# Performance work log

Measured on AMD Instinct MI355X. Metric: run time of the kernel, lower is better.

Reference implementation:

```python
import jax, jax.numpy as jnp
import numpy as np

B, D_IN, D_H = 32768, 512, 512


def setup_inputs() -> dict:
    key = jax.random.key(0)
    ks = jax.random.split(key, 7)
    s_in = 1.0 / np.sqrt(D_IN)
    s_h = 1.0 / np.sqrt(D_H)
    x = jax.random.normal(ks[0], (B, D_IN), dtype=jnp.float32)
    C = jax.random.normal(ks[1], (B, D_H), dtype=jnp.float32)
    h = jax.random.normal(ks[2], (B, D_H), dtype=jnp.float32)
    # Concatenated gate weights: order [i, f, o, g]. Each gate has its own
    # independent Linear(input_dim->hidden) and Linear(hidden->hidden) in torch;
    # stacking them column-wise gives identical math with 2 GEMMs.
    Wx = jax.random.uniform(ks[3], (D_IN, 4 * D_H), dtype=jnp.float32, minval=-s_in, maxval=s_in)
    bx = jax.random.uniform(ks[4], (4 * D_H,), dtype=jnp.float32, minval=-s_in, maxval=s_in)
    Wh = jax.random.uniform(ks[5], (D_H, 4 * D_H), dtype=jnp.float32, minval=-s_h, maxval=s_h)
    bh = jax.random.uniform(ks[6], (4 * D_H,), dtype=jnp.float32, minval=-s_h, maxval=s_h)
    return {"x": x, "C": C, "h": h, "Wx": Wx, "bx": bx, "Wh": Wh, "bh": bh}


def reference(x, C, h, Wx, bx, Wh, bh):
    # Two fused GEMMs replace the 8 small Linear calls (same math).
    z = x @ Wx + bx + h @ Wh + bh  # [B, 4H]
    i, f, o, g = jnp.split(z, 4, axis=-1)
    i = jax.nn.sigmoid(i)
    f = jax.nn.sigmoid(f)
    o = jax.nn.sigmoid(o)
    g = jnp.tanh(g)
    C_new = f * C + i * g
    h_new = o * jnp.tanh(C_new)
    return (C_new, h_new)
```

## Files before the change

### kernel.cpp

```cpp
#include <hip/hip_runtime.h>
#include <stdint.h>


#define BROWS 32768
#define DH 512
#define KTOT 1024
#define BM 128
#define BK 64

typedef __attribute__((ext_vector_type(8))) __bf16 bf16x8;
typedef __attribute__((ext_vector_type(4))) float f32x4;

__device__ __forceinline__ float sigf(float v)  { return 1.0f / (1.0f + __expf(-v)); }
__device__ __forceinline__ float tanhf_(float v){ return 1.0f - 2.0f / (1.0f + __expf(2.0f * v)); }

__global__ void pack_w(const float* __restrict__ Wx, const float* __restrict__ Wh,
                       __bf16* __restrict__ Wt) {
  int o  = blockIdx.x * 256 + threadIdx.x;
  int k  = o & (KTOT - 1);
  int rg = o >> 10;
  int jb = rg >> 7;
  int r  = rg & 127;
  int g  = (r >> 4) & 3;
  int hl = ((r >> 6) << 4) | (r & 15);
  int n  = g * DH + jb * 32 + hl;
  float v = (k < DH) ? Wx[k * 4 * DH + n] : Wh[(k - DH) * 4 * DH + n];
  Wt[o] = (__bf16)v;
}

__global__ __launch_bounds__(256, 3) void lstm_gemm(
    const float* __restrict__ x, const float* __restrict__ h,
    const __bf16* __restrict__ Wt, const float* __restrict__ bx,
    const float* __restrict__ bh, const float* __restrict__ Cin,
    float* __restrict__ out) {
  __shared__ __attribute__((aligned(16))) __bf16 As[BM * BK];
  __shared__ __attribute__((aligned(16))) __bf16 Bs[BM * BK];

  const int tid  = threadIdx.x;
  const int lane = tid & 63;
  const int wave = tid >> 6;
  const int wm = wave >> 1, wn = wave & 1;
  const int jb   = blockIdx.x;
  const int bm   = blockIdx.y;
  const int row0 = bm * BM;

  const __bf16* Bt = Wt + (size_t)jb * 128 * KTOT;

  f32x4 acc[4][4];
  #pragma unroll
  for (int a_ = 0; a_ < 4; ++a_)
    #pragma unroll
    for (int b_ = 0; b_ < 4; ++b_) acc[a_][b_] = (f32x4)0.0f;

  for (int k0 = 0; k0 < KTOT; k0 += BK) {
    const float* Aptr = (k0 < DH) ? (x + (size_t)row0 * DH + k0)
                                  : (h + (size_t)row0 * DH + (k0 - DH));
    bf16x8 ta[4], tb[4];
    #pragma unroll
    for (int it = 0; it < 4; ++it) {
      int lin = it * 256 + tid;
      int r = lin >> 3, c8 = lin & 7;
      const float* src = Aptr + r * DH + c8 * 8;
      float4 f0 = *(const float4*)src;
      float4 f1 = *(const float4*)(src + 4);
      bf16x8 v;
      v[0] = (__bf16)f0.x; v[1] = (__bf16)f0.y;
      v[2] = (__bf16)f0.z; v[3] = (__bf16)f0.w;
      v[4] = (__bf16)f1.x; v[5] = (__bf16)f1.y;
      v[6] = (__bf16)f1.z; v[7] = (__bf16)f1.w;
      ta[it] = v;
    }
    #pragma unroll
    for (int it = 0; it < 4; ++it) {
      int lin = it * 256 + tid;
      int r = lin >> 3, c8 = lin & 7;
      tb[it] = *(const bf16x8*)(Bt + (size_t)r * KTOT + k0 + c8 * 8);
    }
    #pragma unroll
    for (int it = 0; it < 4; ++it) {
      int lin = it * 256 + tid;
      *(bf16x8*)&As[lin * 8] = ta[it];
      *(bf16x8*)&Bs[lin * 8] = tb[it];
    }
    __syncthreads();

    #pragma unroll
    for (int ks = 0; ks < 2; ++ks) {
      const int ko = ks * 32 + (lane >> 4) * 8;
      bf16x8 af[4], bfr[4];
      #pragma unroll
      for (int cm = 0; cm < 4; ++cm)
        af[cm] = *(const bf16x8*)&As[(wm * 64 + cm * 16 + (lane & 15)) * BK + ko];
      #pragma unroll
      for (int cn = 0; cn < 4; ++cn)
        bfr[cn] = *(const bf16x8*)&Bs[(wn * 64 + cn * 16 + (lane & 15)) * BK + ko];
      #pragma unroll
      for (int cm = 0; cm < 4; ++cm)
        #pragma unroll
        for (int cn = 0; cn < 4; ++cn)
          acc[cm][cn] = __builtin_amdgcn_mfma_f32_16x16x32_bf16(
              af[cm], bfr[cn], acc[cm][cn], 0, 0, 0);
    }
    __syncthreads();
  }

  const int hd = jb * 32 + wn * 16 + (lane & 15);
  float bias[4];
  #pragma unroll
  for (int g2 = 0; g2 < 4; ++g2)
    bias[g2] = bx[g2 * DH + hd] + bh[g2 * DH + hd];

  #pragma unroll
  for (int cm = 0; cm < 4; ++cm) {
    const int rbase = row0 + wm * 64 + cm * 16 + (lane >> 4) * 4;
    #pragma unroll
    for (int i2 = 0; i2 < 4; ++i2) {
      const size_t r = (size_t)(rbase + i2);
      float ig = sigf(acc[cm][0][i2] + bias[0]);
      float fg = sigf(acc[cm][1][i2] + bias[1]);
      float og = sigf(acc[cm][2][i2] + bias[2]);
      float gg = tanhf_(acc[cm][3][i2] + bias[3]);
      float cp = Cin[r * DH + hd];
      float cnew = fg * cp + ig * gg;
      float hnew = og * tanhf_(cnew);
      out[r * DH + hd] = cnew;
      out[(size_t)BROWS * DH + r * DH + hd] = hnew;
    }
  }
}

__global__ void lstm_naive(const float* __restrict__ x, const float* __restrict__ Cin,
                           const float* __restrict__ h, const float* __restrict__ Wx,
                           const float* __restrict__ bxp, const float* __restrict__ Wh,
                           const float* __restrict__ bhp, float* __restrict__ out) {
  int idx = blockIdx.x * 256 + threadIdx.x;
  int r = idx >> 9, hd = idx & 511;
  float z[4];
  #pragma unroll
  for (int g = 0; g < 4; ++g)
    z[g] = bxp[g * DH + hd] + bhp[g * DH + hd];
  for (int k = 0; k < DH; ++k) {
    float xv = x[(size_t)r * DH + k];
    #pragma unroll
    for (int g = 0; g < 4; ++g) z[g] += xv * Wx[k * 4 * DH + g * DH + hd];
  }
  for (int k = 0; k < DH; ++k) {
    float hv = h[(size_t)r * DH + k];
    #pragma unroll
    for (int g = 0; g < 4; ++g) z[g] += hv * Wh[k * 4 * DH + g * DH + hd];
  }
  float ig = sigf(z[0]), fg = sigf(z[1]), og = sigf(z[2]), gg = tanhf_(z[3]);
  float cp = Cin[(size_t)r * DH + hd];
  float cnew = fg * cp + ig * gg;
  float hnew = og * tanhf_(cnew);
  out[(size_t)r * DH + hd] = cnew;
  out[(size_t)BROWS * DH + (size_t)r * DH + hd] = hnew;
}

extern "C" void kernel_launch(void* const* d_in, const int* in_sizes, int n_in,
                              void* d_out, int out_size, void* d_ws, size_t ws_size,
                              hipStream_t stream) {
  const float* x  = (const float*)d_in[0];
  const float* Ci = (const float*)d_in[1];
  const float* h  = (const float*)d_in[2];
  const float* Wx = (const float*)d_in[3];
  const float* bx = (const float*)d_in[4];
  const float* Wh = (const float*)d_in[5];
  const float* bh = (const float*)d_in[6];
  float* out = (float*)d_out;

  const size_t need = (size_t)2048 * KTOT * sizeof(__bf16);
  if (ws_size >= need) {
    __bf16* Wt = (__bf16*)d_ws;
    pack_w<<<dim3((2048 * KTOT) / 256), dim3(256), 0, stream>>>(Wx, Wh, Wt);
    lstm_gemm<<<dim3(16, 256), dim3(256), 0, stream>>>(x, h, Wt, bx, bh, Ci, out);
  } else {
    lstm_naive<<<dim3((BROWS * DH) / 256), dim3(256), 0, stream>>>(
        x, Ci, h, Wx, bx, Wh, bh, out);
  }
}
```

Before: 505.0 us.

## Pre-convert activations to bf16 and load GEMM tiles directly into LDS

Adds a pre-pass that converts x and h to one concatenated bf16 buffer. The main GEMM then loads its tiles with global_load_lds straight into an XOR-swizzled LDS layout, which should cut bank conflicts and register staging. Cin is prefetched before the K loop, and pack_w is rewritten with an LDS transpose so its global reads coalesce. The cost is an extra pass that reads fp32 activations and writes a 64MB workspace buffer, and the new path only runs when the workspace is large enough.

```diff
diff --git a/kernel.cpp b/kernel.cpp
--- a/kernel.cpp
+++ b/kernel.cpp
@@ -10,22 +10,154 @@
 
 typedef __attribute__((ext_vector_type(8))) __bf16 bf16x8;
 typedef __attribute__((ext_vector_type(4))) float f32x4;
+typedef __attribute__((address_space(1))) void gvoid;
+typedef __attribute__((address_space(3))) void lvoid;
+
+__device__ __forceinline__ void gl_lds16(const void* g, void* l) {
+  __builtin_amdgcn_global_load_lds((gvoid*)g, (lvoid*)l, 16, 0, 0);
+}
 
 __device__ __forceinline__ float sigf(float v)  { return 1.0f / (1.0f + __expf(-v)); }
 __device__ __forceinline__ float tanhf_(float v){ return 1.0f - 2.0f / (1.0f + __expf(2.0f * v)); }
 
+__global__ void conv_xh(const float* __restrict__ x, const float* __restrict__ h,
+                        __bf16* __restrict__ xh) {
+  int o = blockIdx.x * 256 + threadIdx.x;
+  int c = (o & 127) * 8;
+  int r = o >> 7;
+  const float* src = (c < DH) ? (x + (size_t)r * DH + c)
+                              : (h + (size_t)r * DH + (c - DH));
+  float4 f0 = *(const float4*)src;
+  float4 f1 = *(const float4*)(src + 4);
+  bf16x8 v;
+  v[0] = (__bf16)f0.x; v[1] = (__bf16)f0.y; v[2] = (__bf16)f0.z; v[3] = (__bf16)f0.w;
+  v[4] = (__bf16)f1.x; v[5] = (__bf16)f1.y; v[6] = (__bf16)f1.z; v[7] = (__bf16)f1.w;
+  *(bf16x8*)(xh + (size_t)o * 8) = v;
+}
+
 __global__ void pack_w(const float* __restrict__ Wx, const float* __restrict__ Wh,
                        __bf16* __restrict__ Wt) {
-  int o  = blockIdx.x * 256 + threadIdx.x;
-  int k  = o & (KTOT - 1);
-  int rg = o >> 10;
-  int jb = rg >> 7;
-  int r  = rg & 127;
-  int g  = (r >> 4) & 3;
-  int hl = ((r >> 6) << 4) | (r & 15);
-  int n  = g * DH + jb * 32 + hl;
-  float v = (k < DH) ? Wx[k * 4 * DH + n] : Wh[(k - DH) * 4 * DH + n];
-  Wt[o] = (__bf16)v;
+  __shared__ __bf16 T[128][72];
+  const int jb = blockIdx.y;
+  const int k0 = blockIdx.x * 64;
+  const float* Wsrc = (k0 < DH) ? (Wx + (size_t)k0 * 4 * DH)
+                                : (Wh + (size_t)(k0 - DH) * 4 * DH);
+  const int t = threadIdx.x;
+  const int s = t & 31, kr0 = t >> 5;
+  const int g = s >> 3, q = s & 7;
+  const int r0 = (q >> 2) * 64 + g * 16 + (q & 3) * 4;
+  #pragma unroll
+  for (int it = 0; it < 8; ++it) {
+    int kr = it * 8 + kr0;
+    float4 f = *(const float4*)(Wsrc + (size_t)kr * 4 * DH + g * DH + jb * 32 + q * 4);
+    T[r0 + 0][kr] = (__bf16)f.x;
+    T[r0 + 1][kr] = (__bf16)f.y;
+    T[r0 + 2][kr] = (__bf16)f.z;
+    T[r0 + 3][kr] = (__bf16)f.w;
+  }
+  __syncthreads();
+  #pragma unroll
+  for (int it = 0; it < 4; ++it) {
+    int lin = it * 256 + t;
+    int r = lin >> 3, k8 = lin & 7;
+    bf16x8 v;
+    #pragma unroll
+    for (int j = 0; j < 8; ++j) v[j] = T[r][k8 * 8 + j];
+    *(bf16x8*)(Wt + (size_t)(jb * 128 + r) * KTOT + k0 + k8 * 8) = v;
+  }
+}
+
+__global__ __launch_bounds__(256, 3) void lstm_gemm2(
+    const __bf16* __restrict__ xh, const __bf16* __restrict__ Wt,
+    const float* __restrict__ bx, const float* __restrict__ bh,
+    const float* __restrict__ Cin, float* __restrict__ out) {
+  __shared__ __attribute__((aligned(16))) __bf16 As[BM * BK];
+  __shared__ __attribute__((aligned(16))) __bf16 Bs[BM * BK];
+
+  const int tid  = threadIdx.x;
+  const int lane = tid & 63;
+  const int wave = tid >> 6;
+  const int wm = wave >> 1, wn = wave & 1;
+  const int jb   = blockIdx.x;
+  const int row0 = blockIdx.y * BM;
+
+  const __bf16* Bt = Wt + (size_t)jb * 128 * KTOT;
+
+  const int hd = jb * 32 + wn * 16 + (lane & 15);
+  float bias[4], cpv[4][4];
+  #pragma unroll
+  for (int g = 0; g < 4; ++g) bias[g] = bx[g * DH + hd] + bh[g * DH + hd];
+  #pragma unroll
+  for (int cm = 0; cm < 4; ++cm)
+    #pragma unroll
+    for (int i2 = 0; i2 < 4; ++i2)
+      cpv[cm][i2] = Cin[(size_t)(row0 + wm * 64 + cm * 16 + (lane >> 4) * 4 + i2) * DH + hd];
+
+  f32x4 acc[4][4];
+  #pragma unroll
+  for (int a_ = 0; a_ < 4; ++a_)
+    #pragma unroll
+    for (int b_ = 0; b_ < 4; ++b_) acc[a_][b_] = (f32x4)0.0f;
+
+  for (int k0 = 0; k0 < KTOT; k0 += BK) {
+    #pragma unroll
+    for (int it = 0; it < 4; ++it) {
+      int lin = it * 256 + tid;
+      int r = lin >> 3, c8 = lin & 7;
+      int cs = c8 ^ (r & 7);
+      gl_lds16(xh + (size_t)(row0 + r) * KTOT + k0 + cs * 8, &As[lin * 8]);
+    }
+    #pragma unroll
+    for (int it = 0; it < 4; ++it) {
+      int lin = it * 256 + tid;
+      int r = lin >> 3, c8 = lin & 7;
+      int cs = c8 ^ (r & 7);
+      gl_lds16(Bt + (size_t)r * KTOT + k0 + cs * 8, &Bs[lin * 8]);
+    }
+    __syncthreads();
+
+    #pragma unroll
+    for (int ks = 0; ks < 2; ++ks) {
+      const int q = lane >> 4;
+      bf16x8 af[4], bfr[4];
+      #pragma unroll
+      for (int cm = 0; cm < 4; ++cm) {
+        int row = wm * 64 + cm * 16 + (lane & 15);
+        int cc = (ks * 4 + q) ^ (row & 7);
+        af[cm] = *(const bf16x8*)&As[row * BK + cc * 8];
+      }
+      #pragma unroll
+      for (int cn = 0; cn < 4; ++cn) {
+        int row = wn * 64 + cn * 16 + (lane & 15);
+        int cc = (ks * 4 + q) ^ (row & 7);
+        bfr[cn] = *(const bf16x8*)&Bs[row * BK + cc * 8];
+      }
+      #pragma unroll
+      for (int cm = 0; cm < 4; ++cm)
+        #pragma unroll
+        for (int cn = 0; cn < 4; ++cn)
+          acc[cm][cn] = __builtin_amdgcn_mfma_f32_16x16x32_bf16(
+              af[cm], bfr[cn], acc[cm][cn], 0, 0, 0);
+    }
+    __syncthreads();
+  }
+
+  #pragma unroll
+  for (int cm = 0; cm < 4; ++cm) {
+    const int rbase = row0 + wm * 64 + cm * 16 + (lane >> 4) * 4;
+    #pragma unroll
+    for (int i2 = 0; i2 < 4; ++i2) {
+      const size_t r = (size_t)(rbase + i2);
+      float ig = sigf(acc[cm][0][i2] + bias[0]);
+      float fg = sigf(acc[cm][1][i2] + bias[1]);
+      float og = sigf(acc[cm][2][i2] + bias[2]);
+      float gg = tanhf_(acc[cm][3][i2] + bias[3]);
+      float cnew = fg * cpv[cm][i2] + ig * gg;
+      float hnew = og * tanhf_(cnew);
+      out[r * DH + hd] = cnew;
+      out[(size_t)BROWS * DH + r * DH + hd] = hnew;
+    }
+  }
 }
 
 __global__ __launch_bounds__(256, 3) void lstm_gemm(
@@ -35,23 +167,18 @@
     float* __restrict__ out) {
   __shared__ __attribute__((aligned(16))) __bf16 As[BM * BK];
   __shared__ __attribute__((aligned(16))) __bf16 Bs[BM * BK];
-
   const int tid  = threadIdx.x;
   const int lane = tid & 63;
   const int wave = tid >> 6;
   const int wm = wave >> 1, wn = wave & 1;
   const int jb   = blockIdx.x;
-  const int bm   = blockIdx.y;
-  const int row0 = bm * BM;
-
+  const int row0 = blockIdx.y * BM;
   const __bf16* Bt = Wt + (size_t)jb * 128 * KTOT;
-
   f32x4 acc[4][4];
   #pragma unroll
   for (int a_ = 0; a_ < 4; ++a_)
     #pragma unroll
     for (int b_ = 0; b_ < 4; ++b_) acc[a_][b_] = (f32x4)0.0f;
-
   for (int k0 = 0; k0 < KTOT; k0 += BK) {
     const float* Aptr = (k0 < DH) ? (x + (size_t)row0 * DH + k0)
                                   : (h + (size_t)row0 * DH + (k0 - DH));
@@ -64,16 +191,9 @@
       float4 f0 = *(const float4*)src;
       float4 f1 = *(const float4*)(src + 4);
       bf16x8 v;
-      v[0] = (__bf16)f0.x; v[1] = (__bf16)f0.y;
-      v[2] = (__bf16)f0.z; v[3] = (__bf16)f0.w;
-      v[4] = (__bf16)f1.x; v[5] = (__bf16)f1.y;
-      v[6] = (__bf16)f1.z; v[7] = (__bf16)f1.w;
+      v[0] = (__bf16)f0.x; v[1] = (__bf16)f0.y; v[2] = (__bf16)f0.z; v[3] = (__bf16)f0.w;
+      v[4] = (__bf16)f1.x; v[5] = (__bf16)f1.y; v[6] = (__bf16)f1.z; v[7] = (__bf16)f1.w;
       ta[it] = v;
-    }
-    #pragma unroll
-    for (int it = 0; it < 4; ++it) {
-      int lin = it * 256 + tid;
-      int r = lin >> 3, c8 = lin & 7;
       tb[it] = *(const bf16x8*)(Bt + (size_t)r * KTOT + k0 + c8 * 8);
     }
     #pragma unroll
@@ -83,7 +203,6 @@
       *(bf16x8*)&Bs[lin * 8] = tb[it];
     }
     __syncthreads();
-
     #pragma unroll
     for (int ks = 0; ks < 2; ++ks) {
       const int ko = ks * 32 + (lane >> 4) * 8;
@@ -103,13 +222,10 @@
     }
     __syncthreads();
   }
-
   const int hd = jb * 32 + wn * 16 + (lane & 15);
   float bias[4];
   #pragma unroll
-  for (int g2 = 0; g2 < 4; ++g2)
-    bias[g2] = bx[g2 * DH + hd] + bh[g2 * DH + hd];
-
+  for (int g2 = 0; g2 < 4; ++g2) bias[g2] = bx[g2 * DH + hd] + bh[g2 * DH + hd];
   #pragma unroll
   for (int cm = 0; cm < 4; ++cm) {
     const int rbase = row0 + wm * 64 + cm * 16 + (lane >> 4) * 4;
@@ -137,8 +253,7 @@
   int r = idx >> 9, hd = idx & 511;
   float z[4];
   #pragma unroll
-  for (int g = 0; g < 4; ++g)
-    z[g] = bxp[g * DH + hd] + bhp[g * DH + hd];
+  for (int g = 0; g < 4; ++g) z[g] = bxp[g * DH + hd] + bhp[g * DH + hd];
   for (int k = 0; k < DH; ++k) {
     float xv = x[(size_t)r * DH + k];
     #pragma unroll
@@ -169,11 +284,19 @@
   const float* bh = (const float*)d_in[6];
   float* out = (float*)d_out;
 
-  const size_t need = (size_t)2048 * KTOT * sizeof(__bf16);
-  if (ws_size >= need) {
+  const size_t wt_bytes = (size_t)2048 * KTOT * sizeof(__bf16);
+  const size_t xh_bytes = (size_t)BROWS * KTOT * sizeof(__bf16);
+
+  if (ws_size >= wt_bytes + xh_bytes) {
     __bf16* Wt = (__bf16*)d_ws;
-    pack_w<<<dim3((2048 * KTOT) / 256), dim3(256), 0, stream>>>(Wx, Wh, Wt);
-    lstm_gemm<<<dim3(16, 256), dim3(256), 0, stream>>>(x, h, Wt, bx, bh, Ci, out);
+    __bf16* xh = (__bf16*)((char*)d_ws + wt_bytes);
+    pack_w<<<dim3(16, 16), dim3(256), 0, stream>>>(Wx, Wh, Wt);
+    conv_xh<<<dim3((BROWS * KTOT / 8) / 256), dim3(256), 0, stream>>>(x, h, xh);
+    lstm_gemm2<<<dim3(16, BROWS / BM), dim3(256), 0, stream>>>(xh, Wt, bx, bh, Ci, out);
+  } else if (ws_size >= wt_bytes) {
+    __bf16* Wt = (__bf16*)d_ws;
+    pack_w<<<dim3(16, 16), dim3(256), 0, stream>>>(Wx, Wh, Wt);
+    lstm_gemm<<<dim3(16, BROWS / BM), dim3(256), 0, stream>>>(x, h, Wt, bx, bh, Ci, out);
   } else {
     lstm_naive<<<dim3((BROWS * DH) / 256), dim3(256), 0, stream>>>(
         x, Ci, h, Wx, bx, Wh, bh, out);
```

Result: faster. 429.0 us (-15.1%).
